# Performance work log

Measured on AMD Instinct MI355X. Metric: run time of the kernel, lower is better.

The kernel has to match this reference:

```python
import jax, jax.numpy as jnp
import numpy as np

# video grid and attention geometry (must match init_kwargs)
F_T, H_T, W_T = 4, 32, 32
K = 3                      # kernel_size (odd)
P = K // 2
T = F_T * H_T * W_T        # max_num_tokens = 4096
HEADS = 8
DIM_HEAD = 64
SCALE = DIM_HEAD ** -0.5
DIM = 512
INNER = HEADS * DIM_HEAD


def _build_window_indices():
    # flat token index grid, padded with sentinel T (out-of-range -> zero row after gather)
    idx = np.arange(T).reshape(F_T, H_T, W_T)
    padded = np.full((F_T + 2 * P, H_T + 2 * P, W_T + 2 * P), T, dtype=np.int64)
    padded[P:P + F_T, P:P + H_T, P:P + W_T] = idx
    # [T, K^3] neighborhood indices, kernel offsets in (kf, kh, kw) C-order (matches unfoldNd)
    win = np.lib.stride_tricks.sliding_window_view(padded, (K, K, K)).reshape(T, K ** 3)
    # causal: mask keys whose flat index is strictly in the future of the query
    causal = np.arange(T)[:, None] < win
    causal = np.concatenate([np.zeros((T, 1), dtype=bool), causal], axis=1)  # BOS column never masked
    return jnp.asarray(win), jnp.asarray(causal)

WIN_IDX, CAUSAL_MASK = _build_window_indices()


def setup_inputs() -> dict:
    key = jax.random.key(0)
    k0, k1, k2, k3 = jax.random.split(key, 4)
    n = T  # 1 BOS + (T-1) video tokens; padding logic pads body to exactly T tokens
    x = jax.random.normal(k0, (2, n, DIM), dtype=jnp.float32)
    Wq = jax.random.normal(k1, (DIM, INNER), dtype=jnp.float32) * (DIM ** -0.5)
    Wkv = jax.random.normal(k2, (DIM, 2 * INNER), dtype=jnp.float32) * (DIM ** -0.5)
    Wo = jax.random.normal(k3, (INNER, DIM), dtype=jnp.float32) * (INNER ** -0.5)
    bo = jnp.zeros((DIM,), dtype=jnp.float32)
    return {"x": x, "Wq": Wq, "Wkv": Wkv, "Wo": Wo, "bo": bo}


def _split_heads(t, b):
    # [b, n, h*d] -> [(b*h), n, d]
    n = t.shape[1]
    return t.reshape(b, n, HEADS, DIM_HEAD).transpose(0, 2, 1, 3).reshape(b * HEADS, n, DIM_HEAD)


def reference(x, Wq, Wkv, Wo, bo):
    b, n, _ = x.shape
    tpf = H_T * W_T
    padding = tpf - (n - 1) % tpf  # pads body tokens to a multiple of tokens_per_frame
    x = jnp.pad(x, ((0, 0), (0, padding), (0, 0)))
    q = x @ Wq
    k, v = jnp.split(x @ Wkv, 2, axis=-1)
    q, k, v = (_split_heads(t, b) for t in (q, k, v))
    bh = b * HEADS
    q = q[:, 1:] * SCALE            # drop BOS query; [bh, T, d]
    bos_v = v[:, :1]                # BOS attends only to itself -> its value passes through
    k_bos, k = k[:, :1], k[:, 1:]
    v_bos, v = v[:, :1], v[:, 1:]
    # gather K^3 3D neighborhoods; sentinel index T maps to a zero row
    zero_row = jnp.zeros((bh, 1, DIM_HEAD), dtype=k.dtype)
    k_nb = jnp.concatenate([k, zero_row], axis=1)[:, WIN_IDX]   # [bh, T, K^3, d]
    v_nb = jnp.concatenate([v, zero_row], axis=1)[:, WIN_IDX]
    # prepend global BOS key/value to every window
    k_nb = jnp.concatenate([jnp.broadcast_to(k_bos[:, :, None], (bh, T, 1, DIM_HEAD)), k_nb], axis=2)
    v_nb = jnp.concatenate([jnp.broadcast_to(v_bos[:, :, None], (bh, T, 1, DIM_HEAD)), v_nb], axis=2)
    sim = jnp.einsum('bid,bijd->bij', q, k_nb)                  # [bh, T, K^3+1]
    sim = jnp.where(CAUSAL_MASK[None], -jnp.finfo(sim.dtype).max, sim)
    attn = jax.nn.softmax(sim, axis=-1)
    out = jnp.einsum('bij,bijd->bid', attn, v_nb)               # [bh, T, d]
    out = jnp.concatenate([bos_v, out], axis=1)                 # [bh, T+1, d]
    np_tok = out.shape[1]
    out = out.reshape(b, HEADS, np_tok, DIM_HEAD).transpose(0, 2, 1, 3).reshape(b, np_tok, INNER)
    return (out @ Wo + bo)[:, :n]
```

## Files before the change

kernel.cpp:

```cpp
#include <hip/hip_runtime.h>


#define T_TOK   4096
#define DIM     512
#define NQKV    1536

typedef unsigned short u16;
typedef unsigned int   u32;
typedef unsigned long long u64;
typedef __attribute__((ext_vector_type(8))) short short8;
typedef __attribute__((ext_vector_type(4))) float f32x4;
typedef __attribute__((ext_vector_type(2))) float f32x2;
typedef __attribute__((ext_vector_type(4))) u32 u32x4;

__device__ __forceinline__ u16 f2bf(float f) {
    u32 u = __float_as_uint(f);
    return (u16)((u + 0x7fffu + ((u >> 16) & 1u)) >> 16);
}
__device__ __forceinline__ float b2f(u16 u) {
    return __uint_as_float(((u32)u) << 16);
}
__device__ __forceinline__ float dot2bf(u32 q, u32 k, float c) {
    float r = c;
    asm("v_dot2_f32_bf16 %0, %1, %2, %0" : "+v"(r) : "v"(q), "v"(k));
    return r;
}

__device__ __forceinline__ void gload_lds16(const void* g, void* l) {
    __builtin_amdgcn_global_load_lds(
        (const __attribute__((address_space(1))) void*)g,
        (__attribute__((address_space(3))) void*)l, 16, 0, 0);
}

__global__ void cast_all_kernel(const float4* __restrict__ x,
                                const float* __restrict__ Wq, const float* __restrict__ Wkv,
                                const float* __restrict__ Wo,
                                u16* __restrict__ xb, u16* __restrict__ Wt,
                                u16* __restrict__ Wot) {
    __shared__ float S[64 * 65];
    int blk = blockIdx.x;
    int tid = threadIdx.x;
    if (blk < 4096) {
        int i = blk * 256 + tid;
        float4 v = x[i];
        u64 pack = (u64)f2bf(v.x) | ((u64)f2bf(v.y) << 16) |
                   ((u64)f2bf(v.z) << 32) | ((u64)f2bf(v.w) << 48);
        ((u64*)xb)[i] = pack;
        return;
    }
    int isWo = blk >= 4288;
    int tIdx = isWo ? (blk - 4288) : (blk - 4096);
    int tn = tIdx >> 3, tk = tIdx & 7;
    #pragma unroll
    for (int p = 0; p < 16; ++p) {
        int kl = p * 4 + (tid >> 6), nl = tid & 63;
        int gk = tk * 64 + kl, gn = tn * 64 + nl;
        float v;
        if (isWo)            v = Wo[gk * 512 + gn];
        else if (gn < 512)   v = Wq[gk * 512 + gn];
        else                 v = Wkv[gk * 1024 + (gn - 512)];
        S[kl * 65 + nl] = v;
    }
    __syncthreads();
    u16* dst = isWo ? Wot : Wt;
    #pragma unroll
    for (int p = 0; p < 16; ++p) {
        int nl = p * 4 + (tid >> 6), kl = tid & 63;
        dst[(size_t)(tn * 64 + nl) * 512 + tk * 64 + kl] = f2bf(S[kl * 65 + nl]);
    }
}

template <int BM, int BN, int MODE>
__global__ __launch_bounds__(256)
void gemm_nt(const u16* __restrict__ A, const u16* __restrict__ B,
             void* __restrict__ Cv, const float* __restrict__ bias,
             int lda, int ldb, int ldc) {
    constexpr int K = 512, BK = 32, KSTEPS = K / BK;
    constexpr int ACH = BM * 4;
    constexpr int NCH = (BM + BN) * 4;
    constexpr int NLD = NCH / 256;
    constexpr int ABYTES = BM * 64;
    constexpr int HALF = (BM + BN) * 64;
    constexpr int MI = BM / 32, NJ = BN / 32;
    __shared__ __align__(16) char lds[2 * HALF];
    const int tid  = threadIdx.x;
    const int lane = tid & 63, wave = tid >> 6;
    const int quad = lane >> 4, mrow = lane & 15;
    const int wm = wave >> 1, wn = wave & 1;

    const int nblk = gridDim.x * gridDim.y;
    int lid = blockIdx.y * gridDim.x + blockIdx.x;
    if (!(nblk & 7)) lid = (lid & 7) * (nblk >> 3) + (lid >> 3);
    const int bm = lid / (int)gridDim.x, bn = lid % (int)gridDim.x;

    const char* gptr[NLD];
    char*       lptr[NLD];
    #pragma unroll
    for (int it = 0; it < NLD; ++it) {
        int c   = it * 256 + tid;
        int inB = (c >= ACH);
        int a   = inB ? c - ACH : c;
        int r   = a >> 2;
        int kc  = ((a & 3) - (r >> 1)) & 3;
        int row = (inB ? bn * BN : bm * BM) + r;
        const u16* base = inB ? B : A;
        int ld = inB ? ldb : lda;
        gptr[it] = (const char*)(base + (size_t)row * ld + kc * 8);
        lptr[it] = (char*)lds + (it * 256 + wave * 64) * 16;
    }
    const char* aLds[MI];
    const char* bLds[NJ];
    #pragma unroll
    for (int i = 0; i < MI; ++i) {
        int ra = wm * (BM / 2) + i * 16 + mrow;
        aLds[i] = lds + (ra * 4 + ((quad + (ra >> 1)) & 3)) * 16;
    }
    #pragma unroll
    for (int j = 0; j < NJ; ++j) {
        int rb = wn * (BN / 2) + j * 16 + mrow;
        bLds[j] = lds + ABYTES + (rb * 4 + ((quad + (rb >> 1)) & 3)) * 16;
    }

    f32x4 acc[MI][NJ] = {};
    #pragma unroll
    for (int it = 0; it < NLD; ++it)
        gload_lds16(gptr[it], lptr[it]);

    #pragma unroll
    for (int ks = 0; ks < KSTEPS; ++ks) {
        const int cur = ks & 1;
        if (ks + 1 < KSTEPS) {
            #pragma unroll
            for (int it = 0; it < NLD; ++it)
                gload_lds16(gptr[it] + 2 * (ks + 1) * BK, lptr[it] + (cur ^ 1) * HALF);
            asm volatile("s_waitcnt vmcnt(%0)" :: "i"(NLD) : "memory");
        } else {
            asm volatile("s_waitcnt vmcnt(0)" ::: "memory");
        }
        asm volatile("s_barrier" ::: "memory");

        short8 af[MI], bf[NJ];
        #pragma unroll
        for (int i = 0; i < MI; ++i) af[i] = *(const short8*)(aLds[i] + cur * HALF);
        #pragma unroll
        for (int j = 0; j < NJ; ++j) bf[j] = *(const short8*)(bLds[j] + cur * HALF);
        #pragma unroll
        for (int i = 0; i < MI; ++i)
            #pragma unroll
            for (int j = 0; j < NJ; ++j)
                acc[i][j] = __builtin_amdgcn_mfma_f32_16x16x32_bf16(af[i], bf[j], acc[i][j], 0, 0, 0);
        asm volatile("s_waitcnt lgkmcnt(0)" ::: "memory");
        asm volatile("s_barrier" ::: "memory");
    }

    #pragma unroll
    for (int i = 0; i < MI; ++i) {
        #pragma unroll
        for (int j = 0; j < NJ; ++j) {
            int colg = bn * BN + wn * (BN / 2) + j * 16 + mrow;
            #pragma unroll
            for (int r = 0; r < 4; ++r) {
                int rowg = bm * BM + wm * (BM / 2) + i * 16 + quad * 4 + r;
                if (MODE == 0) {
                    ((u16*)Cv)[(size_t)rowg * ldc + colg] = f2bf(acc[i][j][r]);
                } else {
                    ((float*)Cv)[(size_t)rowg * ldc + colg] = acc[i][j][r] + bias[colg];
                }
            }
        }
    }
}

__global__ __launch_bounds__(256)
void attn_kernel(const u16* __restrict__ QKV, u16* __restrict__ O) {
    __shared__ float Pns[4][64];
    const int wave = threadIdx.x >> 6;
    const int bsw = ((blockIdx.x & 7) << 9) | (blockIdx.x >> 3);
    const int wid  = bsw * 4 + wave;
    const int lane = threadIdx.x & 63;
    const int b  = wid >> 13;
    const int hp = (wid >> 12) & 1;
    const int ti = wid & 4095;
    const size_t baseQ = (size_t)b * T_TOK * NQKV;
    const size_t baseO = (size_t)b * T_TOK * DIM;
    const int hbase = hp * 256;

    if (ti == 0) {
        #pragma unroll
        for (int hd = 0; hd < 4; ++hd)
            O[baseO + hbase + hd * 64 + lane] =
                QKV[baseQ + 1024 + hbase + hd * 64 + lane];
        return;
    }
    const int t = ti - 1;
    const int f = t >> 10, hh = (t >> 5) & 31, ww = t & 31;

    const int j = lane >> 2, g = lane & 3;
    int jm1 = j - 1;
    int dh9 = ((jm1 * 11) >> 5) - 1;
    int dw9 = jm1 - (dh9 + 1) * 3 - 1;
    int df = (j >= 1 && j <= 9) ? -1 : 0;
    int dh = (j >= 1 && j <= 9) ? dh9 : ((j >= 10 && j <= 12) ? -1 : 0);
    int dw = (j >= 1 && j <= 9) ? dw9 :
             ((j >= 10 && j <= 12) ? (j - 11) : ((j == 13) ? -1 : 0));
    int nf = f + df, nh = hh + dh, nw = ww + dw;
    int valid = (nf >= 0) && ((unsigned)nh < 32u) && ((unsigned)nw < 32u)
                && (j >= 1) && (j <= 14);
    int p = valid ? (t + 1 + df * 1024 + dh * 32 + dw) : 0;
    int score_on = valid || (j == 0);

    const u16* qbase = QKV + baseQ + (size_t)(t + 1) * NQKV + hbase + g * 16;
    const u16* kbase = QKV + baseQ + (size_t)p * NQKV + 512 + hbase + g * 16;
    u32x4 qa[4], qb[4], ka[4], kb[4];
    #pragma unroll
    for (int hd = 0; hd < 4; ++hd) {
        qa[hd] = *(const u32x4*)(qbase + hd * 64);
        qb[hd] = *(const u32x4*)(qbase + hd * 64 + 8);
        ka[hd] = *(const u32x4*)(kbase + hd * 64);
        kb[hd] = *(const u32x4*)(kbase + hd * 64 + 8);
    }
    float s[4] = {};
    #pragma unroll
    for (int i = 0; i < 4; ++i)
        #pragma unroll
        for (int hd = 0; hd < 4; ++hd) {
            s[hd] = dot2bf(qa[hd][i], ka[hd][i], s[hd]);
            s[hd] = dot2bf(qb[hd][i], kb[hd][i], s[hd]);
        }
    #pragma unroll
    for (int hd = 0; hd < 4; ++hd) {
        s[hd] += __shfl_xor(s[hd], 1);
        s[hd] += __shfl_xor(s[hd], 2);
        s[hd] *= 0.125f;
        s[hd] = score_on ? s[hd] : -3.0e38f;
    }
    float m[4] = {s[0], s[1], s[2], s[3]};
    #pragma unroll
    for (int off = 4; off <= 32; off <<= 1)
        #pragma unroll
        for (int hd = 0; hd < 4; ++hd)
            m[hd] = fmaxf(m[hd], __shfl_xor(m[hd], off));
    float pe[4], l[4];
    #pragma unroll
    for (int hd = 0; hd < 4; ++hd) {
        pe[hd] = __expf(s[hd] - m[hd]);
        l[hd] = pe[hd];
    }
    #pragma unroll
    for (int off = 4; off <= 32; off <<= 1)
        #pragma unroll
        for (int hd = 0; hd < 4; ++hd)
            l[hd] += __shfl_xor(l[hd], off);
    u32 voff = (u32)p * 3072u;

    if ((lane & 3) == 0) {
        int slot = lane >> 2;
        #pragma unroll
        for (int hd = 0; hd < 4; ++hd)
            Pns[wave][hd * 16 + slot] = pe[hd] * __frcp_rn(l[hd]);
    }
    asm volatile("s_waitcnt lgkmcnt(0)" ::: "memory");

    const float* ptab = &Pns[wave][(lane >> 4) * 16];
    const char* vrow = (const char*)(QKV + baseQ + 1024 + hbase) + lane * 8;
    f32x2 a01 = {0.f, 0.f}, a23 = {0.f, 0.f};
    #pragma unroll
    for (int jj = 0; jj < 15; ++jj) {
        u32 o = (u32)__builtin_amdgcn_readlane((int)voff, jj * 4);
        float pj = ptab[jj];
        u64 v = *(const u64*)(vrow + o);
        u32 lo = (u32)v, hi = (u32)(v >> 32);
        f32x2 p2 = {pj, pj};
        f32x2 v0 = {__uint_as_float(lo << 16), __uint_as_float(lo & 0xffff0000u)};
        f32x2 v1 = {__uint_as_float(hi << 16), __uint_as_float(hi & 0xffff0000u)};
        a01 = __builtin_elementwise_fma(p2, v0, a01);
        a23 = __builtin_elementwise_fma(p2, v1, a23);
    }
    u64 pack = (u64)f2bf(a01.x) | ((u64)f2bf(a01.y) << 16) |
               ((u64)f2bf(a23.x) << 32) | ((u64)f2bf(a23.y) << 48);
    *(u64*)((char*)(O + baseO + (size_t)ti * DIM + hbase) + lane * 8) = pack;
}

extern "C" void kernel_launch(void* const* d_in, const int* in_sizes, int n_in,
                              void* d_out, int out_size, void* d_ws, size_t ws_size,
                              hipStream_t stream) {
    const float* x   = (const float*)d_in[0];
    const float* Wq  = (const float*)d_in[1];
    const float* Wkv = (const float*)d_in[2];
    const float* Wo  = (const float*)d_in[3];
    const float* bo  = (const float*)d_in[4];
    float* out = (float*)d_out;
    char* ws = (char*)d_ws;

    u16* xb  = (u16*)(ws + 0);
    u16* Wt  = (u16*)(ws + 8388608);
    u16* Wot = (u16*)(ws + 9961472);
    u16* QKV = (u16*)(ws + 10485760);
    u16* O   = (u16*)(ws + 0);

    cast_all_kernel<<<dim3(4352), dim3(256), 0, stream>>>(
        (const float4*)x, Wq, Wkv, Wo, xb, Wt, Wot);
    gemm_nt<128, 128, 0><<<dim3(12, 64), dim3(256), 0, stream>>>(
        xb, Wt, (void*)QKV, nullptr, 512, 512, 1536);
    attn_kernel<<<dim3(4096), dim3(256), 0, stream>>>(QKV, O);
    gemm_nt<128, 64, 1><<<dim3(8, 64), dim3(256), 0, stream>>>(
        O, Wot, (void*)out, bo, 512, 512, 512);
}
```

Measured before the change: 129.1 us.

## Fuse fp32-to-bf16 cast of x into QKV GEMM A-operand loading

Removes the separate pass that converted x to bf16 in workspace. The QKV GEMM now loads fp32 x rows into registers, prefetched two k-steps ahead, and converts them with v_cvt_pk_bf16_f32 before writing to LDS. B still streams through direct global-to-LDS loads. This drops one full read/write of x and shrinks the cast kernel, but the GEMM reads twice as many A bytes and does extra conversion work and register staging in its main loop.

```diff
diff --git a/kernel.cpp b/kernel.cpp
--- a/kernel.cpp
+++ b/kernel.cpp
@@ -17,8 +17,10 @@
     u32 u = __float_as_uint(f);
     return (u16)((u + 0x7fffu + ((u >> 16) & 1u)) >> 16);
 }
-__device__ __forceinline__ float b2f(u16 u) {
-    return __uint_as_float(((u32)u) << 16);
+__device__ __forceinline__ u32 cvtpk(float lo, float hi) {
+    u32 r;
+    asm("v_cvt_pk_bf16_f32 %0, %1, %2" : "=v"(r) : "v"(lo), "v"(hi));
+    return r;
 }
 __device__ __forceinline__ float dot2bf(u32 q, u32 k, float c) {
     float r = c;
@@ -32,24 +34,14 @@
         (__attribute__((address_space(3))) void*)l, 16, 0, 0);
 }
 
-__global__ void cast_all_kernel(const float4* __restrict__ x,
-                                const float* __restrict__ Wq, const float* __restrict__ Wkv,
+__global__ void cast_all_kernel(const float* __restrict__ Wq, const float* __restrict__ Wkv,
                                 const float* __restrict__ Wo,
-                                u16* __restrict__ xb, u16* __restrict__ Wt,
-                                u16* __restrict__ Wot) {
+                                u16* __restrict__ Wt, u16* __restrict__ Wot) {
     __shared__ float S[64 * 65];
     int blk = blockIdx.x;
     int tid = threadIdx.x;
-    if (blk < 4096) {
-        int i = blk * 256 + tid;
-        float4 v = x[i];
-        u64 pack = (u64)f2bf(v.x) | ((u64)f2bf(v.y) << 16) |
-                   ((u64)f2bf(v.z) << 32) | ((u64)f2bf(v.w) << 48);
-        ((u64*)xb)[i] = pack;
-        return;
-    }
-    int isWo = blk >= 4288;
-    int tIdx = isWo ? (blk - 4288) : (blk - 4096);
+    int isWo = blk >= 192;
+    int tIdx = isWo ? (blk - 192) : blk;
     int tn = tIdx >> 3, tk = tIdx & 7;
     #pragma unroll
     for (int p = 0; p < 16; ++p) {
@@ -70,9 +62,9 @@
     }
 }
 
-template <int BM, int BN, int MODE>
+template <int BM, int BN, int MODE, int AF32>
 __global__ __launch_bounds__(256)
-void gemm_nt(const u16* __restrict__ A, const u16* __restrict__ B,
+void gemm_nt(const void* __restrict__ Av, const u16* __restrict__ B,
              void* __restrict__ Cv, const float* __restrict__ bias,
              int lda, int ldb, int ldc) {
     constexpr int K = 512, BK = 32, KSTEPS = K / BK;
@@ -93,21 +85,6 @@
     if (!(nblk & 7)) lid = (lid & 7) * (nblk >> 3) + (lid >> 3);
     const int bm = lid / (int)gridDim.x, bn = lid % (int)gridDim.x;
 
-    const char* gptr[NLD];
-    char*       lptr[NLD];
-    #pragma unroll
-    for (int it = 0; it < NLD; ++it) {
-        int c   = it * 256 + tid;
-        int inB = (c >= ACH);
-        int a   = inB ? c - ACH : c;
-        int r   = a >> 2;
-        int kc  = ((a & 3) - (r >> 1)) & 3;
-        int row = (inB ? bn * BN : bm * BM) + r;
-        const u16* base = inB ? B : A;
-        int ld = inB ? ldb : lda;
-        gptr[it] = (const char*)(base + (size_t)row * ld + kc * 8);
-        lptr[it] = (char*)lds + (it * 256 + wave * 64) * 16;
-    }
     const char* aLds[MI];
     const char* bLds[NJ];
     #pragma unroll
@@ -122,35 +99,142 @@
     }
 
     f32x4 acc[MI][NJ] = {};
-    #pragma unroll
-    for (int it = 0; it < NLD; ++it)
-        gload_lds16(gptr[it], lptr[it]);
-
-    #pragma unroll
-    for (int ks = 0; ks < KSTEPS; ++ks) {
-        const int cur = ks & 1;
-        if (ks + 1 < KSTEPS) {
-            #pragma unroll
-            for (int it = 0; it < NLD; ++it)
-                gload_lds16(gptr[it] + 2 * (ks + 1) * BK, lptr[it] + (cur ^ 1) * HALF);
-            asm volatile("s_waitcnt vmcnt(%0)" :: "i"(NLD) : "memory");
-        } else {
-            asm volatile("s_waitcnt vmcnt(0)" ::: "memory");
-        }
-        asm volatile("s_barrier" ::: "memory");
-
-        short8 af[MI], bf[NJ];
-        #pragma unroll
-        for (int i = 0; i < MI; ++i) af[i] = *(const short8*)(aLds[i] + cur * HALF);
-        #pragma unroll
-        for (int j = 0; j < NJ; ++j) bf[j] = *(const short8*)(bLds[j] + cur * HALF);
-        #pragma unroll
-        for (int i = 0; i < MI; ++i)
-            #pragma unroll
-            for (int j = 0; j < NJ; ++j)
-                acc[i][j] = __builtin_amdgcn_mfma_f32_16x16x32_bf16(af[i], bf[j], acc[i][j], 0, 0, 0);
+
+    if constexpr (!AF32) {
+        const u16* A = (const u16*)Av;
+        const char* gptr[NLD];
+        char*       lptr[NLD];
+        #pragma unroll
+        for (int it = 0; it < NLD; ++it) {
+            int c   = it * 256 + tid;
+            int inB = (c >= ACH);
+            int a   = inB ? c - ACH : c;
+            int r   = a >> 2;
+            int kc  = ((a & 3) - (r >> 1)) & 3;
+            int row = (inB ? bn * BN : bm * BM) + r;
+            const u16* base = inB ? B : A;
+            int ld = inB ? ldb : lda;
+            gptr[it] = (const char*)(base + (size_t)row * ld + kc * 8);
+            lptr[it] = (char*)lds + (it * 256 + wave * 64) * 16;
+        }
+        #pragma unroll
+        for (int it = 0; it < NLD; ++it)
+            gload_lds16(gptr[it], lptr[it]);
+
+        #pragma unroll
+        for (int ks = 0; ks < KSTEPS; ++ks) {
+            const int cur = ks & 1;
+            if (ks + 1 < KSTEPS) {
+                #pragma unroll
+                for (int it = 0; it < NLD; ++it)
+                    gload_lds16(gptr[it] + 2 * (ks + 1) * BK, lptr[it] + (cur ^ 1) * HALF);
+                asm volatile("s_waitcnt vmcnt(%0)" :: "i"(NLD) : "memory");
+            } else {
+                asm volatile("s_waitcnt vmcnt(0)" ::: "memory");
+            }
+            asm volatile("s_barrier" ::: "memory");
+
+            short8 af[MI], bf[NJ];
+            #pragma unroll
+            for (int i = 0; i < MI; ++i) af[i] = *(const short8*)(aLds[i] + cur * HALF);
+            #pragma unroll
+            for (int j = 0; j < NJ; ++j) bf[j] = *(const short8*)(bLds[j] + cur * HALF);
+            #pragma unroll
+            for (int i = 0; i < MI; ++i)
+                #pragma unroll
+                for (int j = 0; j < NJ; ++j)
+                    acc[i][j] = __builtin_amdgcn_mfma_f32_16x16x32_bf16(af[i], bf[j], acc[i][j], 0, 0, 0);
+            asm volatile("s_waitcnt lgkmcnt(0)" ::: "memory");
+            asm volatile("s_barrier" ::: "memory");
+        }
+    } else {
+        static_assert(BM == 128 && BN == 128, "AF32 path sized for 128x128");
+        const float* xA = (const float*)Av;
+        const char* gB[2]; char* lB[2];
+        #pragma unroll
+        for (int it = 0; it < 2; ++it) {
+            int a  = it * 256 + tid;
+            int r  = a >> 2;
+            int kc = ((a & 3) - (r >> 1)) & 3;
+            gB[it] = (const char*)(B + (size_t)(bn * BN + r) * ldb + kc * 8);
+            lB[it] = (char*)lds + ABYTES + (it * 256 + wave * 64) * 16;
+        }
+        const float* pA[2];
+        u32 aOff[2];
+        #pragma unroll
+        for (int c = 0; c < 2; ++c) {
+            int a  = c * 256 + tid;
+            int r  = a >> 2;
+            int kc = ((a & 3) - (r >> 1)) & 3;
+            pA[c]   = xA + (size_t)(bm * BM + r) * lda + kc * 8;
+            aOff[c] = (u32)a * 16;
+        }
+
+        float4 aReg[2][2][2];
+        #pragma unroll
+        for (int it = 0; it < 2; ++it)
+            gload_lds16(gB[it], lB[it]);
+        #pragma unroll
+        for (int c = 0; c < 2; ++c)
+            #pragma unroll
+            for (int h = 0; h < 2; ++h)
+                aReg[0][c][h] = *(const float4*)(pA[c] + h * 4);
+        #pragma unroll
+        for (int c = 0; c < 2; ++c)
+            #pragma unroll
+            for (int h = 0; h < 2; ++h)
+                aReg[1][c][h] = *(const float4*)(pA[c] + 32 + h * 4);
+        #pragma unroll
+        for (int c = 0; c < 2; ++c) {
+            float4 v0 = aReg[0][c][0], v1 = aReg[0][c][1];
+            u32x4 w = { cvtpk(v0.x, v0.y), cvtpk(v0.z, v0.w),
+                        cvtpk(v1.x, v1.y), cvtpk(v1.z, v1.w) };
+            *(u32x4*)((char*)lds + aOff[c]) = w;
+        }
         asm volatile("s_waitcnt lgkmcnt(0)" ::: "memory");
-        asm volatile("s_barrier" ::: "memory");
+
+        #pragma unroll
+        for (int ks = 0; ks < KSTEPS; ++ks) {
+            const int cur = ks & 1;
+            if (ks + 1 < KSTEPS) {
+                #pragma unroll
+                for (int it = 0; it < 2; ++it)
+                    gload_lds16(gB[it] + 2 * (ks + 1) * BK, lB[it] + (cur ^ 1) * HALF);
+                if (ks + 2 < KSTEPS) {
+                    #pragma unroll
+                    for (int c = 0; c < 2; ++c)
+                        #pragma unroll
+                        for (int h = 0; h < 2; ++h)
+                            aReg[ks & 1][c][h] = *(const float4*)(pA[c] + (ks + 2) * 32 + h * 4);
+                    asm volatile("s_waitcnt vmcnt(6)" ::: "memory");
+                } else {
+                    asm volatile("s_waitcnt vmcnt(2)" ::: "memory");
+                }
+                #pragma unroll
+                for (int c = 0; c < 2; ++c) {
+                    float4 v0 = aReg[(ks + 1) & 1][c][0], v1 = aReg[(ks + 1) & 1][c][1];
+                    u32x4 w = { cvtpk(v0.x, v0.y), cvtpk(v0.z, v0.w),
+                                cvtpk(v1.x, v1.y), cvtpk(v1.z, v1.w) };
+                    *(u32x4*)((char*)lds + (cur ^ 1) * HALF + aOff[c]) = w;
+                }
+            } else {
+                asm volatile("s_waitcnt vmcnt(0)" ::: "memory");
+            }
+            asm volatile("s_barrier" ::: "memory");
+
+            short8 af[MI], bf[NJ];
+            #pragma unroll
+            for (int i = 0; i < MI; ++i) af[i] = *(const short8*)(aLds[i] + cur * HALF);
+            #pragma unroll
+            for (int j = 0; j < NJ; ++j) bf[j] = *(const short8*)(bLds[j] + cur * HALF);
+            #pragma unroll
+            for (int i = 0; i < MI; ++i)
+                #pragma unroll
+                for (int j = 0; j < NJ; ++j)
+                    acc[i][j] = __builtin_amdgcn_mfma_f32_16x16x32_bf16(af[i], bf[j], acc[i][j], 0, 0, 0);
+            asm volatile("s_waitcnt lgkmcnt(0)" ::: "memory");
+            asm volatile("s_barrier" ::: "memory");
+        }
     }
 
     #pragma unroll
@@ -292,17 +376,15 @@
     float* out = (float*)d_out;
     char* ws = (char*)d_ws;
 
-    u16* xb  = (u16*)(ws + 0);
     u16* Wt  = (u16*)(ws + 8388608);
     u16* Wot = (u16*)(ws + 9961472);
     u16* QKV = (u16*)(ws + 10485760);
     u16* O   = (u16*)(ws + 0);
 
-    cast_all_kernel<<<dim3(4352), dim3(256), 0, stream>>>(
-        (const float4*)x, Wq, Wkv, Wo, xb, Wt, Wot);
-    gemm_nt<128, 128, 0><<<dim3(12, 64), dim3(256), 0, stream>>>(
-        xb, Wt, (void*)QKV, nullptr, 512, 512, 1536);
+    cast_all_kernel<<<dim3(256), dim3(256), 0, stream>>>(Wq, Wkv, Wo, Wt, Wot);
+    gemm_nt<128, 128, 0, 1><<<dim3(12, 64), dim3(256), 0, stream>>>(
+        (const void*)x, Wt, (void*)QKV, nullptr, 512, 512, 1536);
     attn_kernel<<<dim3(4096), dim3(256), 0, stream>>>(QKV, O);
-    gemm_nt<128, 64, 1><<<dim3(8, 64), dim3(256), 0, stream>>>(
-        O, Wot, (void*)out, bo, 512, 512, 512);
-}
+    gemm_nt<128, 64, 1, 0><<<dim3(8, 64), dim3(256), 0, stream>>>(
+        (const void*)O, Wot, (void*)out, bo, 512, 512, 512);
+}
```

Result: no change. 127.7 us (-1.1%).
